# Kernel optimization log

Hardware: AMD Instinct MI355X
Metric: run time of the kernel (lower is better)

Reference implementation:

```python
import jax, jax.numpy as jnp
import numpy as np

D_MODEL = 256
NUM_WAVES = 8192
NUM_TRANSITIONS = 8192
NUM_TARGETS = 4096
BATCH = 4
TOP_K = 3


def setup_inputs() -> dict:
    key = jax.random.key(0)
    ks = jax.random.split(key, 16)
    d = D_MODEL
    inp = {
        'wave': jax.random.normal(ks[0], (BATCH, NUM_WAVES, d), jnp.float32),
        'transition': jax.random.normal(ks[1], (BATCH, NUM_TRANSITIONS, d), jnp.float32),
        'target': jax.random.normal(ks[2], (BATCH, NUM_TARGETS, d), jnp.float32),
        # learned adjacency logits (init: randn * 0.1)
        'w2t_adj': jax.random.normal(ks[3], (NUM_WAVES, NUM_TRANSITIONS), jnp.float32) * 0.1,
        't2t_adj': jax.random.normal(ks[4], (NUM_TRANSITIONS, NUM_TARGETS), jnp.float32) * 0.1,
        'temperature': jnp.array(1.0, jnp.float32),
        # gumbel noise (fixed sample, as drawn inside F.gumbel_softmax)
        'g_wt': jax.random.gumbel(ks[5], (NUM_WAVES, NUM_TRANSITIONS), jnp.float32),
        'g_tt': jax.random.gumbel(ks[6], (NUM_TRANSITIONS, NUM_TARGETS), jnp.float32),
        # wave->transition edge-weight predictor MLP: Linear(2d,d) ReLU Linear(d,1) Sigmoid
        'wt_w1': jax.random.normal(ks[7], (2 * d, d), jnp.float32) / np.sqrt(2 * d),
        'wt_b1': jnp.zeros((d,), jnp.float32),
        'wt_w2': jax.random.normal(ks[8], (d, 1), jnp.float32) / np.sqrt(d),
        'wt_b2': jnp.zeros((1,), jnp.float32),
        # transition->target predictor MLP
        'tt_w1': jax.random.normal(ks[9], (2 * d, d), jnp.float32) / np.sqrt(2 * d),
        'tt_b1': jnp.zeros((d,), jnp.float32),
        'tt_w2': jax.random.normal(ks[10], (d, 1), jnp.float32) / np.sqrt(d),
        'tt_b2': jnp.zeros((1,), jnp.float32),
    }
    return inp


def _gumbel_softmax(logits, gumbel_noise, tau):
    return jax.nn.softmax((logits + gumbel_noise) / tau, axis=-1)


def _generate_edges(probs, src_feat, tgt_feat, w1, b1, w2, b2):
    # probs: [S, T]; src_feat: [B, S, d]; tgt_feat: [B, T, d]
    S = probs.shape[0]
    top_vals, top_idx = jax.lax.top_k(probs, TOP_K)  # [S, k]
    src_idx = jnp.broadcast_to(jnp.arange(S)[:, None], (S, TOP_K)).reshape(-1)  # [S*k]
    tgt_idx = top_idx.reshape(-1)                                               # [S*k]
    edge_index = jnp.stack([src_idx, tgt_idx])                                  # [2, S*k]
    # gather node features of batch element 0 (as in the original code)
    e_src = src_feat[0][src_idx]                                                # [S*k, d]
    e_tgt = tgt_feat[0][tgt_idx]                                                # [S*k, d]
    e = jnp.concatenate([e_src, e_tgt], axis=-1)                                # [S*k, 2d]
    h = jax.nn.relu(e @ w1 + b1)
    mlp_w = jax.nn.sigmoid(h @ w2 + b2)[:, 0]                                   # [S*k]
    final_w = mlp_w * top_vals.reshape(-1)
    return edge_index, final_w


def reference(wave, transition, target, w2t_adj, t2t_adj, temperature,
              g_wt, g_tt, wt_w1, wt_b1, wt_w2, wt_b2,
              tt_w1, tt_b1, tt_w2, tt_b2):
    # training=True path: gumbel-softmax (soft) over adjacency logits
    wt_probs = _gumbel_softmax(w2t_adj, g_wt, temperature)
    tt_probs = _gumbel_softmax(t2t_adj, g_tt, temperature)
    wt_edges, wt_weights = _generate_edges(wt_probs, wave, transition,
                                           wt_w1, wt_b1, wt_w2, wt_b2)
    tt_edges, tt_weights = _generate_edges(tt_probs, transition, target,
                                           tt_w1, tt_b1, tt_w2, tt_b2)
    return wt_edges, wt_weights, tt_edges, tt_weights
```

## Files before the change

### kernel.cpp

```cpp
#include <hip/hip_runtime.h>

#define NWAVES 8192
#define NTRANS 8192
#define NTGT   4096
#define DMODEL 256
#define TOPK   3
#define EW (NWAVES * TOPK)
#define ET (NTRANS * TOPK)

struct GemmLds {
    float As[32][68];
    float Bs[32][64];
};

template<int NCOLS>
__device__ __forceinline__ void topk_wave_body(int row, int lane,
        const float* __restrict__ adj, const float* __restrict__ gum, float inv_tau,
        float* __restrict__ out_src, float* __restrict__ out_tgt,
        int* __restrict__ ws_idx, float* __restrict__ ws_val)
{
    constexpr int NIT = NCOLS / 256;
    const float4* ap = reinterpret_cast<const float4*>(adj + (size_t)row * NCOLS) + lane;
    const float4* gp = reinterpret_cast<const float4*>(gum + (size_t)row * NCOLS) + lane;
    const int lane4 = lane * 4;

    float av0 = -1e30f, av1 = -1e30f, av2 = -1e30f; int ai0 = 0, ai1 = 0, ai2 = 0;
    float bv0 = -1e30f, bv1 = -1e30f, bv2 = -1e30f; int bi0 = 0, bi1 = 0, bi2 = 0;
    float s0 = 0.f, s1 = 0.f, s2 = 0.f, s3 = 0.f;

    auto insA = [&](float z, int c) {
        const bool g0 = z > av0, g1 = z > av1, g2 = z > av2;
        av2 = __builtin_amdgcn_fmed3f(z, av1, av2);
        ai2 = g1 ? ai1 : (g2 ? c : ai2);
        av1 = __builtin_amdgcn_fmed3f(z, av0, av1);
        ai1 = g0 ? ai0 : (g1 ? c : ai1);
        av0 = fmaxf(z, av0);
        ai0 = g0 ? c : ai0;
    };
    auto insB = [&](float z, int c) {
        const bool g0 = z > bv0, g1 = z > bv1, g2 = z > bv2;
        bv2 = __builtin_amdgcn_fmed3f(z, bv1, bv2);
        bi2 = g1 ? bi1 : (g2 ? c : bi2);
        bv1 = __builtin_amdgcn_fmed3f(z, bv0, bv1);
        bi1 = g0 ? bi0 : (g1 ? c : bi1);
        bv0 = fmaxf(z, bv0);
        bi0 = g0 ? c : bi0;
    };
    auto proc = [&](const float4& a, const float4& g, int it) {
        const int cb = it * 256 + lane4;
        const float za = fmaf(a.x + g.x, inv_tau, -10.0f);
        const float zb = fmaf(a.y + g.y, inv_tau, -10.0f);
        const float zc = fmaf(a.z + g.z, inv_tau, -10.0f);
        const float zd = fmaf(a.w + g.w, inv_tau, -10.0f);
        s0 += __expf(za); s1 += __expf(zb); s2 += __expf(zc); s3 += __expf(zd);
        insA(za, cb); insA(zb, cb | 1); insB(zc, cb | 2); insB(zd, cb | 3);
    };

    float4 A0 = ap[0 * 64], A1 = ap[1 * 64], A2 = ap[2 * 64], A3 = ap[3 * 64];
    float4 G0 = gp[0 * 64], G1 = gp[1 * 64], G2 = gp[2 * 64], G3 = gp[3 * 64];
#pragma unroll
    for (int it = 0; it < NIT; it += 4) {
        const bool more = (it + 4) < NIT;
        proc(A0, G0, it + 0);
        if (more) { A0 = ap[(it + 4) * 64]; G0 = gp[(it + 4) * 64]; }
        proc(A1, G1, it + 1);
        if (more) { A1 = ap[(it + 5) * 64]; G1 = gp[(it + 5) * 64]; }
        proc(A2, G2, it + 2);
        if (more) { A2 = ap[(it + 6) * 64]; G2 = gp[(it + 6) * 64]; }
        proc(A3, G3, it + 3);
        if (more) { A3 = ap[(it + 7) * 64]; G3 = gp[(it + 7) * 64]; }
    }

    auto insIA = [&](float z, int c) {
        const bool e0 = (z == av0), e1 = (z == av1), e2 = (z == av2);
        const bool g0 = (z > av0) || (e0 && c < ai0);
        const bool g1 = (z > av1) || (e1 && c < ai1);
        const bool g2 = (z > av2) || (e2 && c < ai2);
        av2 = __builtin_amdgcn_fmed3f(z, av1, av2);
        ai2 = g1 ? ai1 : (g2 ? c : ai2);
        av1 = __builtin_amdgcn_fmed3f(z, av0, av1);
        ai1 = g0 ? ai0 : (g1 ? c : ai1);
        av0 = fmaxf(z, av0);
        ai0 = g0 ? c : ai0;
    };

    insIA(bv0, bi0); insIA(bv1, bi1); insIA(bv2, bi2);
    float s = (s0 + s1) + (s2 + s3);

#pragma unroll
    for (int m = 1; m < 64; m <<= 1) {
        const float u0 = __shfl_xor(av0, m), u1 = __shfl_xor(av1, m), u2 = __shfl_xor(av2, m);
        const int   j0 = __shfl_xor(ai0, m), j1 = __shfl_xor(ai1, m), j2 = __shfl_xor(ai2, m);
        s += __shfl_xor(s, m);
        insIA(u0, j0); insIA(u1, j1); insIA(u2, j2);
    }

    if (lane == 0) {
        const float invS = 1.0f / s;
        const size_t e = (size_t)row * TOPK;
        out_src[e] = (float)row; out_src[e + 1] = (float)row; out_src[e + 2] = (float)row;
        out_tgt[e] = (float)ai0; out_tgt[e + 1] = (float)ai1; out_tgt[e + 2] = (float)ai2;
        ws_idx[e] = ai0; ws_idx[e + 1] = ai1; ws_idx[e + 2] = ai2;
        ws_val[e] = __expf(av0) * invS;
        ws_val[e + 1] = __expf(av1) * invS;
        ws_val[e + 2] = __expf(av2) * invS;
    }
}

__device__ __forceinline__ void gemm_body(void* ldsraw,
        const float* __restrict__ A, const float* __restrict__ B,
        float* __restrict__ C, int m0, int n0)
{
    GemmLds& L = *reinterpret_cast<GemmLds*>(ldsraw);
    const int tid = threadIdx.x;
    const int tx = tid % 16, ty = tid / 16;
    const int lc = tid % 32;
    const int lr = tid / 32;
    const int bn = tid % 64;
    const int bk = tid / 64;
    float acc[4][4] = {};

    for (int k0 = 0; k0 < DMODEL; k0 += 32) {
#pragma unroll
        for (int i = 0; i < 8; ++i) {
            const int r = lr + i * 8;
            L.As[lc][r] = A[(size_t)(m0 + r) * DMODEL + k0 + lc];
        }
#pragma unroll
        for (int i = 0; i < 8; ++i) {
            const int kk = bk + i * 4;
            L.Bs[kk][bn] = B[(size_t)(k0 + kk) * DMODEL + n0 + bn];
        }
        __syncthreads();
#pragma unroll
        for (int kk = 0; kk < 32; ++kk) {
            const float4 a4 = *reinterpret_cast<const float4*>(&L.As[kk][ty * 4]);
            const float4 b4 = *reinterpret_cast<const float4*>(&L.Bs[kk][tx * 4]);
            const float av[4] = {a4.x, a4.y, a4.z, a4.w};
            const float bv[4] = {b4.x, b4.y, b4.z, b4.w};
#pragma unroll
            for (int i = 0; i < 4; ++i)
#pragma unroll
                for (int j = 0; j < 4; ++j)
                    acc[i][j] += av[i] * bv[j];
        }
        __syncthreads();
    }
#pragma unroll
    for (int i = 0; i < 4; ++i) {
        float4 c4 = {acc[i][0], acc[i][1], acc[i][2], acc[i][3]};
        *reinterpret_cast<float4*>(&C[(size_t)(m0 + ty * 4 + i) * DMODEL + n0 + tx * 4]) = c4;
    }
}

__global__ __launch_bounds__(256)
void fused_main_kernel(const float* __restrict__ w2t, const float* __restrict__ g_wt,
                       const float* __restrict__ t2t, const float* __restrict__ g_tt,
                       const float* __restrict__ temp,
                       const float* __restrict__ wave, const float* __restrict__ trans,
                       const float* __restrict__ target,
                       const float* __restrict__ wt_w1, const float* __restrict__ tt_w1,
                       float* wt_src, float* wt_tgt, int* wt_idx, float* wt_val,
                       float* tt_src, float* tt_tgt, int* tt_idx, float* tt_val,
                       float* AW, float* BW, float* AT, float* BT,
                       int nGemm)
{
    __shared__ alignas(16) unsigned char ldsraw[sizeof(GemmLds)];
    const int bid = blockIdx.x;

    int topk_id = -1, gemm_id = -1;
    if (nGemm > 0) {
        const int inter = nGemm * 3;
        if (bid < inter) {
            if (bid % 3 == 0) gemm_id = bid / 3;
            else topk_id = bid - bid / 3 - 1;
        } else {
            topk_id = bid - nGemm;
        }
    } else {
        topk_id = bid;
    }

    if (gemm_id >= 0) {
        const float* A; const float* B; float* C; int mblk, nblk;
        if (gemm_id < 512)       { A = wave;   B = wt_w1;                    C = AW; int g = gemm_id;        mblk = g % 128; nblk = g / 128; }
        else if (gemm_id < 1024) { A = trans;  B = wt_w1 + DMODEL * DMODEL;  C = BW; int g = gemm_id - 512;  mblk = g % 128; nblk = g / 128; }
        else if (gemm_id < 1536) { A = trans;  B = tt_w1;                    C = AT; int g = gemm_id - 1024; mblk = g % 128; nblk = g / 128; }
        else                     { A = target; B = tt_w1 + DMODEL * DMODEL;  C = BT; int g = gemm_id - 1536; mblk = g % 64;  nblk = g / 64;  }
        gemm_body(ldsraw, A, B, C, mblk * 64, nblk * 64);
        return;
    }

    const int lane = threadIdx.x & 63;
    const int wv = threadIdx.x >> 6;
    const int row = topk_id * 4 + wv;
    const float inv_tau = 1.0f / temp[0];
    if (row < NWAVES)
        topk_wave_body<NTRANS>(row, lane, w2t, g_wt, inv_tau, wt_src, wt_tgt, wt_idx, wt_val);
    else
        topk_wave_body<NTGT>(row - NWAVES, lane, t2t, g_tt, inv_tau, tt_src, tt_tgt, tt_idx, tt_val);
}

__global__ __launch_bounds__(256)
void edge_weight_fused_kernel(const float* __restrict__ AW, const float* __restrict__ BW,
                              const float* __restrict__ AT, const float* __restrict__ BT,
                              const int* __restrict__ wt_idx, const float* __restrict__ wt_val,
                              const int* __restrict__ tt_idx, const float* __restrict__ tt_val,
                              const float* __restrict__ wt_b1, const float* __restrict__ wt_w2, const float* __restrict__ wt_b2,
                              const float* __restrict__ tt_b1, const float* __restrict__ tt_w2, const float* __restrict__ tt_b2,
                              float* __restrict__ wt_out, float* __restrict__ tt_out)
{
    const int lane = threadIdx.x & 63;
    const int wv   = threadIdx.x >> 6;
    const int eg = blockIdx.x * 4 + wv;

    const bool isWT = (eg < EW);
    const int e = isWT ? eg : eg - EW;
    const float* Arows = isWT ? AW : AT;
    const float* Brows = isWT ? BW : BT;
    const int*   eidx  = isWT ? wt_idx : tt_idx;
    const float* evals = isWT ? wt_val : tt_val;
    const float* b1    = isWT ? wt_b1 : tt_b1;
    const float* w2    = isWT ? wt_w2 : tt_w2;
    const float* b2    = isWT ? wt_b2 : tt_b2;
    float*       outw  = isWT ? wt_out : tt_out;

    const int srow = e / 3;
    const int trow = eidx[e];
    const float4 a4 = *reinterpret_cast<const float4*>(Arows + (size_t)srow * DMODEL + lane * 4);
    const float4 b4 = *reinterpret_cast<const float4*>(Brows + (size_t)trow * DMODEL + lane * 4);
    const float4 c4 = *reinterpret_cast<const float4*>(b1 + lane * 4);
    const float4 w4 = *reinterpret_cast<const float4*>(w2 + lane * 4);
    float acc = fmaxf(a4.x + b4.x + c4.x, 0.f) * w4.x
              + fmaxf(a4.y + b4.y + c4.y, 0.f) * w4.y
              + fmaxf(a4.z + b4.z + c4.z, 0.f) * w4.z
              + fmaxf(a4.w + b4.w + c4.w, 0.f) * w4.w;
#pragma unroll
    for (int off = 32; off >= 1; off >>= 1) acc += __shfl_xor(acc, off);
    if (lane == 0) {
        const float x = acc + b2[0];
        const float sig = 1.0f / (1.0f + __expf(-x));
        outw[e] = sig * evals[e];
    }
}

__global__ __launch_bounds__(256)
void edge_mlp_direct_kernel(const float* __restrict__ src_feat,
                            const float* __restrict__ tgt_feat,
                            const int* __restrict__ eidx,
                            const float* __restrict__ evals,
                            const float* __restrict__ w1,
                            const float* __restrict__ b1,
                            const float* __restrict__ w2,
                            const float* __restrict__ b2,
                            float* __restrict__ out_w,
                            int nEdges)
{
    __shared__ float E[512][16];
    __shared__ float part[16][4];
    const int tid = threadIdx.x;
    const int e0 = blockIdx.x * 16;

    for (int i = tid; i < 16 * 128; i += 256) {
        const int e = i >> 7;
        const int q = i & 127;
        const int eg = e0 + e;
        float4 v;
        if (eg < nEdges) {
            if (q < 64) {
                const float* r = src_feat + (size_t)(eg / 3) * DMODEL;
                v = *reinterpret_cast<const float4*>(r + q * 4);
            } else {
                const float* r = tgt_feat + (size_t)eidx[eg] * DMODEL;
                v = *reinterpret_cast<const float4*>(r + (q - 64) * 4);
            }
        } else {
            v = make_float4(0.f, 0.f, 0.f, 0.f);
        }
        const int k = q * 4;
        E[k + 0][e] = v.x; E[k + 1][e] = v.y; E[k + 2][e] = v.z; E[k + 3][e] = v.w;
    }
    __syncthreads();

    const int j = tid;
    float acc[16];
#pragma unroll
    for (int e = 0; e < 16; ++e) acc[e] = 0.f;

    for (int k = 0; k < 512; ++k) {
        const float w = w1[(size_t)k * DMODEL + j];
        const float4 a = *reinterpret_cast<const float4*>(&E[k][0]);
        const float4 b = *reinterpret_cast<const float4*>(&E[k][4]);
        const float4 c = *reinterpret_cast<const float4*>(&E[k][8]);
        const float4 d = *reinterpret_cast<const float4*>(&E[k][12]);
        acc[0] += a.x * w;  acc[1] += a.y * w;  acc[2] += a.z * w;  acc[3] += a.w * w;
        acc[4] += b.x * w;  acc[5] += b.y * w;  acc[6] += b.z * w;  acc[7] += b.w * w;
        acc[8] += c.x * w;  acc[9] += c.y * w;  acc[10] += c.z * w; acc[11] += c.w * w;
        acc[12] += d.x * w; acc[13] += d.y * w; acc[14] += d.z * w; acc[15] += d.w * w;
    }

    const float b1j = b1[j];
    const float w2j = w2[j];
    const int lane = tid & 63;
    const int wv = tid >> 6;
#pragma unroll
    for (int e = 0; e < 16; ++e) {
        float v = fmaxf(acc[e] + b1j, 0.f) * w2j;
#pragma unroll
        for (int off = 32; off >= 1; off >>= 1) v += __shfl_xor(v, off);
        if (lane == 0) part[e][wv] = v;
    }
    __syncthreads();
    if (tid < 16) {
        const int eg = e0 + tid;
        if (eg < nEdges) {
            const float x = part[tid][0] + part[tid][1] + part[tid][2] + part[tid][3] + b2[0];
            const float sig = 1.0f / (1.0f + __expf(-x));
            out_w[eg] = sig * evals[eg];
        }
    }
}

extern "C" void kernel_launch(void* const* d_in, const int* in_sizes, int n_in,
                              void* d_out, int out_size, void* d_ws, size_t ws_size,
                              hipStream_t stream)
{
    const float* wave   = (const float*)d_in[0];
    const float* trans  = (const float*)d_in[1];
    const float* target = (const float*)d_in[2];
    const float* w2t    = (const float*)d_in[3];
    const float* t2t    = (const float*)d_in[4];
    const float* temp   = (const float*)d_in[5];
    const float* g_wt   = (const float*)d_in[6];
    const float* g_tt   = (const float*)d_in[7];
    const float* wt_w1  = (const float*)d_in[8];
    const float* wt_b1  = (const float*)d_in[9];
    const float* wt_w2  = (const float*)d_in[10];
    const float* wt_b2  = (const float*)d_in[11];
    const float* tt_w1  = (const float*)d_in[12];
    const float* tt_b1  = (const float*)d_in[13];
    const float* tt_w2  = (const float*)d_in[14];
    const float* tt_b2  = (const float*)d_in[15];

    float* out = (float*)d_out;
    float* wt_src = out;
    float* wt_tgt = out + EW;
    float* wt_wgt = out + 2 * EW;
    float* tt_src = out + 3 * EW;
    float* tt_tgt = out + 3 * EW + ET;
    float* tt_wgt = out + 3 * EW + 2 * ET;

    const size_t nodeFloats = (size_t)(NWAVES + NTRANS + NTRANS + NTGT) * DMODEL;
    const size_t edgeFloats = (size_t)(EW + ET);
    const size_t needBig = (nodeFloats + 2 * edgeFloats) * sizeof(float) + 2 * edgeFloats * sizeof(int);
    const bool bigPath = (ws_size >= needBig);

    float *AW = nullptr, *BW = nullptr, *AT = nullptr, *BT = nullptr;
    float *wt_val, *tt_val; int *wt_idx, *tt_idx;
    if (bigPath) {
        AW = (float*)d_ws;
        BW = AW + NWAVES * DMODEL;
        AT = BW + NTRANS * DMODEL;
        BT = AT + NTRANS * DMODEL;
        wt_val = BT + NTGT * DMODEL;
        tt_val = wt_val + EW;
        wt_idx = (int*)(tt_val + ET);
        tt_idx = wt_idx + EW;
    } else {
        wt_val = (float*)d_ws;
        tt_val = wt_val + EW;
        wt_idx = (int*)(tt_val + ET);
        tt_idx = wt_idx + EW;
    }

    const int nTopkBlocks = (NWAVES + NTRANS) / 4;
    const int nGemm = bigPath ? (512 * 3 + 256) : 0;
    const int grid = nTopkBlocks + nGemm;

    fused_main_kernel<<<grid, 256, 0, stream>>>(
        w2t, g_wt, t2t, g_tt, temp, wave, trans, target, wt_w1, tt_w1,
        wt_src, wt_tgt, wt_idx, wt_val, tt_src, tt_tgt, tt_idx, tt_val,
        AW, BW, AT, BT, nGemm);

    if (bigPath) {
        edge_weight_fused_kernel<<<(EW + ET) / 4, 256, 0, stream>>>(
            AW, BW, AT, BT, wt_idx, wt_val, tt_idx, tt_val,
            wt_b1, wt_w2, wt_b2, tt_b1, tt_w2, tt_b2, wt_wgt, tt_wgt);
    } else {
        edge_mlp_direct_kernel<<<(EW + 15) / 16, 256, 0, stream>>>(wave,  trans,  wt_idx, wt_val, wt_w1, wt_b1, wt_w2, wt_b2, wt_wgt, EW);
        edge_mlp_direct_kernel<<<(ET + 15) / 16, 256, 0, stream>>>(trans, target, tt_idx, tt_val, tt_w1, tt_b1, tt_w2, tt_b2, tt_wgt, ET);
    }
}
```

Measured before the change: 204.2 us.

## Process each top-k row with a full block and nontemporal streaming loads

The top-k/softmax pass now gives each adjacency row to a whole 256-thread block instead of one wave. Each wave's partial top-3 and partial exp-sum are merged through LDS by one thread after a barrier. The adjacency and gumbel rows are read with nontemporal loads, since each value is streamed once. The GEMM/top-k interleave ratio is changed to match the larger number of top-k blocks. This aims to raise memory-level parallelism per row and to keep streamed data from polluting the cache, at the cost of an extra block barrier and a serial LDS merge per row.

Measured after the change: 213.4 us. 4.5% more time.

```diff
diff --git a/kernel.cpp b/kernel.cpp
--- a/kernel.cpp
+++ b/kernel.cpp
@@ -8,21 +8,24 @@
 #define EW (NWAVES * TOPK)
 #define ET (NTRANS * TOPK)
 
+typedef float vf4 __attribute__((ext_vector_type(4)));
+
 struct GemmLds {
     float As[32][68];
     float Bs[32][64];
 };
 
 template<int NCOLS>
-__device__ __forceinline__ void topk_wave_body(int row, int lane,
+__device__ __forceinline__ void topk_block_body(float* lds, int row,
         const float* __restrict__ adj, const float* __restrict__ gum, float inv_tau,
         float* __restrict__ out_src, float* __restrict__ out_tgt,
         int* __restrict__ ws_idx, float* __restrict__ ws_val)
 {
-    constexpr int NIT = NCOLS / 256;
-    const float4* ap = reinterpret_cast<const float4*>(adj + (size_t)row * NCOLS) + lane;
-    const float4* gp = reinterpret_cast<const float4*>(gum + (size_t)row * NCOLS) + lane;
-    const int lane4 = lane * 4;
+    constexpr int NSTEP = NCOLS / 1024;
+    const int tid = threadIdx.x;
+    const vf4* ap = reinterpret_cast<const vf4*>(adj + (size_t)row * NCOLS) + tid;
+    const vf4* gp = reinterpret_cast<const vf4*>(gum + (size_t)row * NCOLS) + tid;
+    const int tid4 = tid * 4;
 
     float av0 = -1e30f, av1 = -1e30f, av2 = -1e30f; int ai0 = 0, ai1 = 0, ai2 = 0;
     float bv0 = -1e30f, bv1 = -1e30f, bv2 = -1e30f; int bi0 = 0, bi1 = 0, bi2 = 0;
@@ -46,8 +49,8 @@
         bv0 = fmaxf(z, bv0);
         bi0 = g0 ? c : bi0;
     };
-    auto proc = [&](const float4& a, const float4& g, int it) {
-        const int cb = it * 256 + lane4;
+    auto proc = [&](vf4 a, vf4 g, int s) {
+        const int cb = s * 1024 + tid4;
         const float za = fmaf(a.x + g.x, inv_tau, -10.0f);
         const float zb = fmaf(a.y + g.y, inv_tau, -10.0f);
         const float zc = fmaf(a.z + g.z, inv_tau, -10.0f);
@@ -56,19 +59,25 @@
         insA(za, cb); insA(zb, cb | 1); insB(zc, cb | 2); insB(zd, cb | 3);
     };
 
-    float4 A0 = ap[0 * 64], A1 = ap[1 * 64], A2 = ap[2 * 64], A3 = ap[3 * 64];
-    float4 G0 = gp[0 * 64], G1 = gp[1 * 64], G2 = gp[2 * 64], G3 = gp[3 * 64];
-#pragma unroll
-    for (int it = 0; it < NIT; it += 4) {
-        const bool more = (it + 4) < NIT;
-        proc(A0, G0, it + 0);
-        if (more) { A0 = ap[(it + 4) * 64]; G0 = gp[(it + 4) * 64]; }
-        proc(A1, G1, it + 1);
-        if (more) { A1 = ap[(it + 5) * 64]; G1 = gp[(it + 5) * 64]; }
-        proc(A2, G2, it + 2);
-        if (more) { A2 = ap[(it + 6) * 64]; G2 = gp[(it + 6) * 64]; }
-        proc(A3, G3, it + 3);
-        if (more) { A3 = ap[(it + 7) * 64]; G3 = gp[(it + 7) * 64]; }
+    vf4 Ab0 = __builtin_nontemporal_load(ap + 0 * 256);
+    vf4 Gb0 = __builtin_nontemporal_load(gp + 0 * 256);
+    vf4 Ab1 = __builtin_nontemporal_load(ap + 1 * 256);
+    vf4 Gb1 = __builtin_nontemporal_load(gp + 1 * 256);
+    vf4 Ab2 = __builtin_nontemporal_load(ap + 2 * 256);
+    vf4 Gb2 = __builtin_nontemporal_load(gp + 2 * 256);
+    vf4 Ab3 = __builtin_nontemporal_load(ap + 3 * 256);
+    vf4 Gb3 = __builtin_nontemporal_load(gp + 3 * 256);
+#pragma unroll
+    for (int s = 0; s < NSTEP; s += 4) {
+        const bool more = (s + 4) < NSTEP;
+        proc(Ab0, Gb0, s + 0);
+        if (more) { Ab0 = __builtin_nontemporal_load(ap + (s + 4) * 256); Gb0 = __builtin_nontemporal_load(gp + (s + 4) * 256); }
+        proc(Ab1, Gb1, s + 1);
+        if (more) { Ab1 = __builtin_nontemporal_load(ap + (s + 5) * 256); Gb1 = __builtin_nontemporal_load(gp + (s + 5) * 256); }
+        proc(Ab2, Gb2, s + 2);
+        if (more) { Ab2 = __builtin_nontemporal_load(ap + (s + 6) * 256); Gb2 = __builtin_nontemporal_load(gp + (s + 6) * 256); }
+        proc(Ab3, Gb3, s + 3);
+        if (more) { Ab3 = __builtin_nontemporal_load(ap + (s + 7) * 256); Gb3 = __builtin_nontemporal_load(gp + (s + 7) * 256); }
     }
 
     auto insIA = [&](float z, int c) {
@@ -95,15 +104,46 @@
         insIA(u0, j0); insIA(u1, j1); insIA(u2, j2);
     }
 
+    float* lv   = lds;
+    int*   li   = (int*)(lds + 12);
+    float* lsum = lds + 24;
+    const int lane = tid & 63, wv = tid >> 6;
     if (lane == 0) {
-        const float invS = 1.0f / s;
+        lv[wv * 3 + 0] = av0; lv[wv * 3 + 1] = av1; lv[wv * 3 + 2] = av2;
+        li[wv * 3 + 0] = ai0; li[wv * 3 + 1] = ai1; li[wv * 3 + 2] = ai2;
+        lsum[wv] = s;
+    }
+    __syncthreads();
+    if (tid == 0) {
+        float v0 = -1e30f, v1 = -1e30f, v2 = -1e30f; int j0 = 0, j1 = 0, j2 = 0;
+        float S = 0.f;
+#pragma unroll
+        for (int w = 0; w < 4; ++w) {
+            S += lsum[w];
+#pragma unroll
+            for (int q = 0; q < 3; ++q) {
+                const float z = lv[w * 3 + q];
+                const int c = li[w * 3 + q];
+                const bool e0 = (z == v0), e1 = (z == v1), e2 = (z == v2);
+                const bool g0 = (z > v0) || (e0 && c < j0);
+                const bool g1 = (z > v1) || (e1 && c < j1);
+                const bool g2 = (z > v2) || (e2 && c < j2);
+                v2 = __builtin_amdgcn_fmed3f(z, v1, v2);
+                j2 = g1 ? j1 : (g2 ? c : j2);
+                v1 = __builtin_amdgcn_fmed3f(z, v0, v1);
+                j1 = g0 ? j0 : (g1 ? c : j1);
+                v0 = fmaxf(z, v0);
+                j0 = g0 ? c : j0;
+            }
+        }
+        const float invS = 1.0f / S;
         const size_t e = (size_t)row * TOPK;
         out_src[e] = (float)row; out_src[e + 1] = (float)row; out_src[e + 2] = (float)row;
-        out_tgt[e] = (float)ai0; out_tgt[e + 1] = (float)ai1; out_tgt[e + 2] = (float)ai2;
-        ws_idx[e] = ai0; ws_idx[e + 1] = ai1; ws_idx[e + 2] = ai2;
-        ws_val[e] = __expf(av0) * invS;
-        ws_val[e + 1] = __expf(av1) * invS;
-        ws_val[e + 2] = __expf(av2) * invS;
+        out_tgt[e] = (float)j0;  out_tgt[e + 1] = (float)j1;  out_tgt[e + 2] = (float)j2;
+        ws_idx[e] = j0; ws_idx[e + 1] = j1; ws_idx[e + 2] = j2;
+        ws_val[e] = __expf(v0) * invS;
+        ws_val[e + 1] = __expf(v1) * invS;
+        ws_val[e + 2] = __expf(v2) * invS;
     }
 }
 
@@ -170,10 +210,10 @@
 
     int topk_id = -1, gemm_id = -1;
     if (nGemm > 0) {
-        const int inter = nGemm * 3;
+        const int inter = nGemm * 10;
         if (bid < inter) {
-            if (bid % 3 == 0) gemm_id = bid / 3;
-            else topk_id = bid - bid / 3 - 1;
+            if (bid % 10 == 0) gemm_id = bid / 10;
+            else topk_id = bid - bid / 10 - 1;
         } else {
             topk_id = bid - nGemm;
         }
@@ -191,14 +231,12 @@
         return;
     }
 
-    const int lane = threadIdx.x & 63;
-    const int wv = threadIdx.x >> 6;
-    const int row = topk_id * 4 + wv;
     const float inv_tau = 1.0f / temp[0];
-    if (row < NWAVES)
-        topk_wave_body<NTRANS>(row, lane, w2t, g_wt, inv_tau, wt_src, wt_tgt, wt_idx, wt_val);
+    float* lds = reinterpret_cast<float*>(ldsraw);
+    if (topk_id < NWAVES)
+        topk_block_body<NTRANS>(lds, topk_id, w2t, g_wt, inv_tau, wt_src, wt_tgt, wt_idx, wt_val);
     else
-        topk_wave_body<NTGT>(row - NWAVES, lane, t2t, g_tt, inv_tau, tt_src, tt_tgt, tt_idx, tt_val);
+        topk_block_body<NTGT>(lds, topk_id - NWAVES, t2t, g_tt, inv_tau, tt_src, tt_tgt, tt_idx, tt_val);
 }
 
 __global__ __launch_bounds__(256)
@@ -373,7 +411,7 @@
         tt_idx = wt_idx + EW;
     }
 
-    const int nTopkBlocks = (NWAVES + NTRANS) / 4;
+    const int nTopkBlocks = NWAVES + NTRANS;
     const int nGemm = bigPath ? (512 * 3 + 256) : 0;
     const int grid = nTopkBlocks + nGemm;
 
```
